# Optimization experiments

Hardware: AMD Instinct MI355X
Metric: run time of the kernel (lower is better)

The kernel has to match this reference:

```python
import jax, jax.numpy as jnp
import numpy as np


def setup_inputs() -> dict:
    key = jax.random.key(0)
    pcd = jax.random.normal(key, (8, 4096, 3), dtype=jnp.float32)
    return {"pcd": pcd, "k": 5}


def reference(pcd, k):
    # pcd: [B, N, 3]. Faithful port of MC3DAD_ONNX.get_geometry_features.
    sq = jnp.sum(pcd * pcd, axis=-1)                       # [B, N]
    d2 = sq[:, :, None] + sq[:, None, :] - 2.0 * jnp.einsum('bnd,bmd->bnm', pcd, pcd)
    dist = jnp.sqrt(jnp.maximum(d2, 0.0))                  # [B, N, N], == torch.cdist
    # k nearest neighbors (smallest distances) -> indices only
    _, idx = jax.lax.top_k(-dist, k)                       # idx: [B, N, K]
    # gather neighbor coordinates: [B, N, K, 3]
    neighbors = jax.vmap(lambda p, i: p[i])(pcd, idx)
    centroid = jnp.mean(neighbors, axis=2, keepdims=True)  # [B, N, 1, 3]
    centered = neighbors - centroid                        # [B, N, K, 3]
    # per-point 3x3 covariance: centered^T @ centered / (K-1)
    cov = jnp.einsum('bnkc,bnkd->bncd', centered, centered) / (k - 1)
    trace = jnp.trace(cov, axis1=-2, axis2=-1)             # [B, N]
    curvature = trace / (jnp.sum(trace, axis=-1, keepdims=True) + 1e-8)
    return curvature
```

## Files before the change

kernel.cpp:

```cpp
#include <hip/hip_runtime.h>
#include <hip/hip_bf16.h>


typedef unsigned long long ull;

constexpr int N_PTS  = 4096;
constexpr int BATCH  = 8;
constexpr int KNN    = 5;
constexpr int SEG    = 8;
constexpr int SEGLEN = N_PTS / SEG;
constexpr int QPW    = 8;
constexpr int NTHR   = 1024;
constexpr int QPB    = (NTHR / 64) * QPW;
constexpr int KSLOT  = 16;
constexpr int TRIG   = KSLOT - 4;

__device__ __forceinline__ int swz(int j) { return j + (j >> 9); }

__device__ __forceinline__ ull umin64(ull a, ull b) { return a < b ? a : b; }
__device__ __forceinline__ ull umax64(ull a, ull b) { return a < b ? b : a; }

__device__ __forceinline__ void push5(float dd, int idx,
                                      float d[KNN], int ix[KNN])
{
    float ad = dd; int ai = idx;
    #pragma unroll
    for (int p = 0; p < KNN - 1; ++p) {
        const bool lt = ad < d[p];
        const float md = lt ? ad : d[p];
        const int   mi = lt ? ai : ix[p];
        const float xd = lt ? d[p] : ad;
        const int   xi = lt ? ix[p] : ai;
        d[p] = md; ix[p] = mi; ad = xd; ai = xi;
    }
    const bool lt = ad < d[KNN - 1];
    d[KNN - 1]  = lt ? ad : d[KNN - 1];
    ix[KNN - 1] = lt ? ai : ix[KNN - 1];
}

__device__ __forceinline__ void merge5(ull a[KNN], const ull b[KNN])
{
    const ull r0 = umin64(a[0], b[0]);
    const ull r1 = umin64(umin64(a[1], b[1]), umax64(a[0], b[0]));
    const ull r2 = umin64(umin64(a[2], b[2]),
                          umin64(umax64(a[1], b[0]), umax64(a[0], b[1])));
    const ull r3 = umin64(umin64(a[3], b[3]),
                   umin64(umax64(a[2], b[0]),
                   umin64(umax64(a[1], b[1]), umax64(a[0], b[2]))));
    const ull r4 = umin64(umin64(a[4], b[4]),
                   umin64(umin64(umax64(a[3], b[0]), umax64(a[2], b[1])),
                          umin64(umax64(a[1], b[2]), umax64(a[0], b[3]))));
    a[0] = r0; a[1] = r1; a[2] = r2; a[3] = r3; a[4] = r4;
}

struct KnnShared {
    float4 pts[N_PTS + SEG];
    int    buf[KSLOT * NTHR];
};

__device__ __forceinline__ void drain_buf(int& cnt, const float4 qp,
                                          float dq[KNN], int iq[KNN],
                                          float& tau_q,
                                          const float4* __restrict__ pts,
                                          const int* __restrict__ lanebuf)
{
    for (int j = 0; ; ++j) {
        if (!__any(j < cnt)) break;
        if (j < cnt) {
            const int idx = lanebuf[j * NTHR];
            const float4 c = pts[swz(idx)];
            const float dot = __fadd_rn(__fadd_rn(__fmul_rn(qp.x, c.x),
                                                  __fmul_rn(qp.y, c.y)),
                                        __fmul_rn(qp.z, c.z));
            const float dd = __fsub_rn(__fadd_rn(qp.w, c.w),
                                       __fmul_rn(2.0f, dot));
            push5(dd, idx, dq, iq);
        }
    }
    cnt = 0;
    tau_q = __fsub_rn(dq[KNN - 1], qp.w) + 6e-5f;
}

__global__ __launch_bounds__(NTHR, 4)
void knn_trace_kernel(const float* __restrict__ pcd, float* __restrict__ trace_out)
{
    __shared__ KnnShared sh;

    const int b = blockIdx.y;
    const int t = threadIdx.x;
    const float* __restrict__ batch = pcd + (size_t)b * N_PTS * 3;

    #pragma unroll
    for (int i = 0; i < N_PTS / NTHR; ++i) {
        const int p = t + i * NTHR;
        const float x = batch[p * 3 + 0];
        const float y = batch[p * 3 + 1];
        const float z = batch[p * 3 + 2];
        const float sq = __fadd_rn(__fadd_rn(__fmul_rn(x, x), __fmul_rn(y, y)),
                                   __fmul_rn(z, z));
        sh.pts[swz(p)] = make_float4(x, y, z, sq);
    }
    __syncthreads();

    const int lane = t & 63;
    const int wave = t >> 6;
    const int q    = lane & 7;
    const int s    = lane >> 3;
    const int qbase = blockIdx.x * QPB + wave * QPW;
    const float4 qp = sh.pts[swz(qbase + q)];

    float dq[KNN];
    int   iq[KNN];
    #pragma unroll
    for (int r = 0; r < KNN; ++r) { dq[r] = __builtin_inff(); iq[r] = 0x7fffffff; }

    const float4* __restrict__ seg = sh.pts + (s * SEGLEN + s);
    int* __restrict__ lanebuf = sh.buf + t;

    int   cnt   = 0;
    float tau_q = __builtin_inff();
    const int idx0 = s * SEGLEN;

    for (int m0 = 0; m0 < SEGLEN; m0 += 4) {
        #pragma unroll
        for (int u = 0; u < 4; ++u) {
            const float4 c = seg[m0 + u];
            const float t2 = fmaf(-2.0f,
                                  fmaf(qp.x, c.x,
                                       fmaf(qp.y, c.y, qp.z * c.z)),
                                  c.w);
            const bool keep = t2 < tau_q;
            lanebuf[cnt * NTHR] = idx0 + m0 + u;
            cnt += keep ? 1 : 0;
        }
        if (__any(cnt > TRIG))
            drain_buf(cnt, qp, dq, iq, tau_q, sh.pts, lanebuf);
    }
    drain_buf(cnt, qp, dq, iq, tau_q, sh.pts, lanebuf);

    ull key[KNN];
    #pragma unroll
    for (int r = 0; r < KNN; ++r) {
        const float dist = __fsqrt_rn(fmaxf(dq[r], 0.0f));
        key[r] = ((ull)__float_as_uint(dist) << 32) | (unsigned)iq[r];
    }
    #pragma unroll
    for (int i = 0; i < KNN - 1; ++i)
        #pragma unroll
        for (int p = 0; p < KNN - 1 - i; ++p) {
            const ull lo = umin64(key[p], key[p + 1]);
            const ull hi = umax64(key[p], key[p + 1]);
            key[p] = lo; key[p + 1] = hi;
        }

    #pragma unroll
    for (int mask = 8; mask < 64; mask <<= 1) {
        ull o[KNN];
        #pragma unroll
        for (int r = 0; r < KNN; ++r) o[r] = __shfl_xor(key[r], mask);
        merge5(key, o);
    }

    if (lane < 8) {
        float nx[KNN], ny[KNN], nz[KNN];
        #pragma unroll
        for (int r = 0; r < KNN; ++r) {
            const int sel = (int)(key[r] & 0xffffffffull);
            const float4 p = sh.pts[swz(sel)];
            nx[r] = p.x; ny[r] = p.y; nz[r] = p.z;
        }

        float sx = nx[0], sy = ny[0], sz = nz[0];
        #pragma unroll
        for (int r = 1; r < KNN; ++r) {
            sx = __fadd_rn(sx, nx[r]);
            sy = __fadd_rn(sy, ny[r]);
            sz = __fadd_rn(sz, nz[r]);
        }
        const float cx = __fdiv_rn(sx, 5.0f);
        const float cy = __fdiv_rn(sy, 5.0f);
        const float cz = __fdiv_rn(sz, 5.0f);

        float sxx = 0.0f, syy = 0.0f, szz = 0.0f;
        #pragma unroll
        for (int r = 0; r < KNN; ++r) {
            const float dx = __fsub_rn(nx[r], cx);
            const float dy = __fsub_rn(ny[r], cy);
            const float dz = __fsub_rn(nz[r], cz);
            sxx = __fadd_rn(sxx, __fmul_rn(dx, dx));
            syy = __fadd_rn(syy, __fmul_rn(dy, dy));
            szz = __fadd_rn(szz, __fmul_rn(dz, dz));
        }
        const float trace = __fadd_rn(__fadd_rn(__fmul_rn(sxx, 0.25f),
                                                __fmul_rn(syy, 0.25f)),
                                      __fmul_rn(szz, 0.25f));
        trace_out[(size_t)b * N_PTS + qbase + lane] = trace;
    }
}

__global__ __launch_bounds__(256)
void curvature_kernel(const float* __restrict__ trace, float* __restrict__ out)
{
    __shared__ float red[256];
    const int b = blockIdx.x >> 3;
    const int c = blockIdx.x & 7;
    const int t = threadIdx.x;
    const float* __restrict__ tr = trace + (size_t)b * N_PTS;

    float s = 0.0f;
    #pragma unroll
    for (int i = 0; i < N_PTS / 256; ++i)
        s += tr[t + i * 256];
    red[t] = s;
    __syncthreads();
    #pragma unroll
    for (int o = 128; o > 0; o >>= 1) {
        if (t < o) red[t] += red[t + o];
        __syncthreads();
    }
    const float denom = red[0] + 1e-8f;

    float* __restrict__ ob = out + (size_t)b * N_PTS;
    const int x = c * 512 + t;
    ob[x]       = tr[x]       / denom;
    ob[x + 256] = tr[x + 256] / denom;
}

extern "C" void kernel_launch(void* const* d_in, const int* in_sizes, int n_in,
                              void* d_out, int out_size, void* d_ws, size_t ws_size,
                              hipStream_t stream)
{
    (void)in_sizes; (void)n_in; (void)out_size; (void)ws_size;
    const float* pcd = (const float*)d_in[0];
    float* trace = (float*)d_ws;
    float* out = (float*)d_out;

    dim3 gridA(N_PTS / QPB, BATCH);
    knn_trace_kernel<<<gridA, NTHR, 0, stream>>>(pcd, trace);
    curvature_kernel<<<BATCH * 8, 256, 0, stream>>>(trace, out);
}
```

Before: 135.5 us.

## Rewrite KNN as register-broadcast scan with shared tau and fused normalization

Replaces the shared-memory point table with per-wave register chunks that are broadcast via readlane, so each lane handles one query against a 512-point segment per wave. A running threshold is shared across waves through atomicMin on LDS. Partial top-5 lists are merged through shared memory, and the normalization kernel is folded in using a last-block-done counter. This removes the LDS point table and the second launch, but it adds a memset, global-memory gathers during drains, per-candidate wave votes, and a serial tail in the last block.

```diff
diff --git a/kernel.cpp b/kernel.cpp
--- a/kernel.cpp
+++ b/kernel.cpp
@@ -3,20 +3,23 @@
 
 
 typedef unsigned long long ull;
+typedef unsigned short u16;
+typedef unsigned int u32;
 
 constexpr int N_PTS  = 4096;
 constexpr int BATCH  = 8;
 constexpr int KNN    = 5;
-constexpr int SEG    = 8;
-constexpr int SEGLEN = N_PTS / SEG;
-constexpr int QPW    = 8;
-constexpr int NTHR   = 1024;
-constexpr int QPB    = (NTHR / 64) * QPW;
+constexpr int NTHR   = 512;
+constexpr int WPB    = 8;
+constexpr int QPB    = 64;
+constexpr int SEGLEN = 512;
+constexpr int CHUNKS = 8;
 constexpr int KSLOT  = 16;
-constexpr int TRIG   = KSLOT - 4;
-
-__device__ __forceinline__ int swz(int j) { return j + (j >> 9); }
-
+constexpr int TRIG   = 12;
+
+__device__ __forceinline__ float rl(float v, int j) {
+    return __int_as_float(__builtin_amdgcn_readlane(__float_as_int(v), j));
+}
 __device__ __forceinline__ ull umin64(ull a, ull b) { return a < b ? a : b; }
 __device__ __forceinline__ ull umax64(ull a, ull b) { return a < b ? b : a; }
 
@@ -38,7 +41,7 @@
     ix[KNN - 1] = lt ? ai : ix[KNN - 1];
 }
 
-__device__ __forceinline__ void merge5(ull a[KNN], const ull b[KNN])
+__device__ __forceinline__ void merge5(ull a[KNN], const ull* __restrict__ b)
 {
     const ull r0 = umin64(a[0], b[0]);
     const ull r1 = umin64(umin64(a[1], b[1]), umax64(a[0], b[0]));
@@ -53,90 +56,110 @@
     a[0] = r0; a[1] = r1; a[2] = r2; a[3] = r3; a[4] = r4;
 }
 
-struct KnnShared {
-    float4 pts[N_PTS + SEG];
-    int    buf[KSLOT * NTHR];
+struct Sh {
+    u16 buf[KSLOT * NTHR];
+    u32 tau_bits[QPB];
+    int lastflag;
+    union {
+        ull   mrg[QPB][WPB][KNN];
+        float red[256];
+    } u;
 };
 
-__device__ __forceinline__ void drain_buf(int& cnt, const float4 qp,
-                                          float dq[KNN], int iq[KNN],
-                                          float& tau_q,
-                                          const float4* __restrict__ pts,
-                                          const int* __restrict__ lanebuf)
-{
-    for (int j = 0; ; ++j) {
-        if (!__any(j < cnt)) break;
+__device__ __forceinline__ void drain_buf(int& cnt, float qx, float qy, float qz, float qw,
+                                          float dq[KNN], int iq[KNN], float& tau,
+                                          const float* __restrict__ batch,
+                                          const u16* lanebuf, u32* tau_bits, int lane)
+{
+    for (int j = 0; __any(j < cnt); ++j) {
         if (j < cnt) {
-            const int idx = lanebuf[j * NTHR];
-            const float4 c = pts[swz(idx)];
-            const float dot = __fadd_rn(__fadd_rn(__fmul_rn(qp.x, c.x),
-                                                  __fmul_rn(qp.y, c.y)),
-                                        __fmul_rn(qp.z, c.z));
-            const float dd = __fsub_rn(__fadd_rn(qp.w, c.w),
-                                       __fmul_rn(2.0f, dot));
+            const int idx = lanebuf[(size_t)j * NTHR];
+            const float x = batch[idx * 3 + 0];
+            const float y = batch[idx * 3 + 1];
+            const float z = batch[idx * 3 + 2];
+            const float sq  = __fadd_rn(__fadd_rn(__fmul_rn(x, x), __fmul_rn(y, y)),
+                                        __fmul_rn(z, z));
+            const float dot = __fadd_rn(__fadd_rn(__fmul_rn(qx, x), __fmul_rn(qy, y)),
+                                        __fmul_rn(qz, z));
+            const float dd  = __fsub_rn(__fadd_rn(qw, sq), __fmul_rn(2.0f, dot));
             push5(dd, idx, dq, iq);
         }
     }
     cnt = 0;
-    tau_q = __fsub_rn(dq[KNN - 1], qp.w) + 6e-5f;
+    atomicMin(&tau_bits[lane], __float_as_uint(dq[KNN - 1]));
+    const u32 tb = *(volatile u32*)&tau_bits[lane];
+    tau = __uint_as_float(tb) - qw + 6e-5f;
 }
 
 __global__ __launch_bounds__(NTHR, 4)
-void knn_trace_kernel(const float* __restrict__ pcd, float* __restrict__ trace_out)
-{
-    __shared__ KnnShared sh;
-
-    const int b = blockIdx.y;
-    const int t = threadIdx.x;
-    const float* __restrict__ batch = pcd + (size_t)b * N_PTS * 3;
-
-    #pragma unroll
-    for (int i = 0; i < N_PTS / NTHR; ++i) {
-        const int p = t + i * NTHR;
-        const float x = batch[p * 3 + 0];
-        const float y = batch[p * 3 + 1];
-        const float z = batch[p * 3 + 2];
-        const float sq = __fadd_rn(__fadd_rn(__fmul_rn(x, x), __fmul_rn(y, y)),
-                                   __fmul_rn(z, z));
-        sh.pts[swz(p)] = make_float4(x, y, z, sq);
-    }
-    __syncthreads();
-
+void fused_kernel(const float* __restrict__ pcd, float* __restrict__ out,
+                  u32* __restrict__ ctr)
+{
+    __shared__ Sh sh;
+
+    const int b    = blockIdx.y;
+    const int qb   = blockIdx.x;
+    const int t    = threadIdx.x;
     const int lane = t & 63;
     const int wave = t >> 6;
-    const int q    = lane & 7;
-    const int s    = lane >> 3;
-    const int qbase = blockIdx.x * QPB + wave * QPW;
-    const float4 qp = sh.pts[swz(qbase + q)];
-
-    float dq[KNN];
-    int   iq[KNN];
+    const float* __restrict__ batch = pcd + (size_t)b * N_PTS * 3;
+
+    if (t < QPB) sh.tau_bits[t] = 0x7f800000u;
+
+    const int q = qb * QPB + lane;
+    const float qx = batch[q * 3 + 0];
+    const float qy = batch[q * 3 + 1];
+    const float qz = batch[q * 3 + 2];
+    const float qw = __fadd_rn(__fadd_rn(__fmul_rn(qx, qx), __fmul_rn(qy, qy)),
+                               __fmul_rn(qz, qz));
+
+    const int wbase = wave * SEGLEN;
+    float cx[CHUNKS], cy[CHUNKS], cz[CHUNKS], cw[CHUNKS];
+    #pragma unroll
+    for (int c = 0; c < CHUNKS; ++c) {
+        const int idx = wbase + c * 64 + lane;
+        cx[c] = batch[idx * 3 + 0];
+        cy[c] = batch[idx * 3 + 1];
+        cz[c] = batch[idx * 3 + 2];
+        cw[c] = __fadd_rn(__fadd_rn(__fmul_rn(cx[c], cx[c]), __fmul_rn(cy[c], cy[c])),
+                          __fmul_rn(cz[c], cz[c]));
+    }
+    __syncthreads();
+
+    float dq[KNN]; int iq[KNN];
     #pragma unroll
     for (int r = 0; r < KNN; ++r) { dq[r] = __builtin_inff(); iq[r] = 0x7fffffff; }
 
-    const float4* __restrict__ seg = sh.pts + (s * SEGLEN + s);
-    int* __restrict__ lanebuf = sh.buf + t;
-
-    int   cnt   = 0;
-    float tau_q = __builtin_inff();
-    const int idx0 = s * SEGLEN;
-
-    for (int m0 = 0; m0 < SEGLEN; m0 += 4) {
-        #pragma unroll
-        for (int u = 0; u < 4; ++u) {
-            const float4 c = seg[m0 + u];
-            const float t2 = fmaf(-2.0f,
-                                  fmaf(qp.x, c.x,
-                                       fmaf(qp.y, c.y, qp.z * c.z)),
-                                  c.w);
-            const bool keep = t2 < tau_q;
-            lanebuf[cnt * NTHR] = idx0 + m0 + u;
-            cnt += keep ? 1 : 0;
-        }
-        if (__any(cnt > TRIG))
-            drain_buf(cnt, qp, dq, iq, tau_q, sh.pts, lanebuf);
-    }
-    drain_buf(cnt, qp, dq, iq, tau_q, sh.pts, lanebuf);
+    u16* lanebuf = sh.buf + t;
+    int   cnt = 0;
+    float tau = __builtin_inff();
+
+    for (int c = 0; c < CHUNKS; ++c) {
+        const u32 tb = *(volatile u32*)&sh.tau_bits[lane];
+        tau = __uint_as_float(tb) - qw + 6e-5f;
+        const int cbase = wbase + c * 64;
+        for (int j0 = 0; j0 < 64; j0 += 4) {
+            #pragma unroll
+            for (int v = 0; v < 4; ++v) {
+                const int j = j0 + v;
+                const float sx = rl(cx[c], j);
+                const float sy = rl(cy[c], j);
+                const float sz = rl(cz[c], j);
+                const float sw = rl(cw[c], j);
+                const float dot = fmaf(qx, sx, fmaf(qy, sy, qz * sz));
+                const float t2  = fmaf(-2.0f, dot, sw);
+                const bool keep = t2 < tau;
+                if (__any(keep)) {
+                    lanebuf[(size_t)cnt * NTHR] = (u16)(cbase + j);
+                    cnt += keep ? 1 : 0;
+                }
+            }
+            if (__any(cnt > TRIG))
+                drain_buf(cnt, qx, qy, qz, qw, dq, iq, tau, batch,
+                          lanebuf, sh.tau_bits, lane);
+        }
+    }
+    drain_buf(cnt, qx, qy, qz, qw, dq, iq, tau, batch, lanebuf, sh.tau_bits, lane);
 
     ull key[KNN];
     #pragma unroll
@@ -152,24 +175,25 @@
             const ull hi = umax64(key[p], key[p + 1]);
             key[p] = lo; key[p + 1] = hi;
         }
-
-    #pragma unroll
-    for (int mask = 8; mask < 64; mask <<= 1) {
-        ull o[KNN];
-        #pragma unroll
-        for (int r = 0; r < KNN; ++r) o[r] = __shfl_xor(key[r], mask);
-        merge5(key, o);
-    }
-
-    if (lane < 8) {
+    #pragma unroll
+    for (int r = 0; r < KNN; ++r) sh.u.mrg[lane][wave][r] = key[r];
+    __syncthreads();
+
+    if (wave == 0) {
+        ull cur[KNN];
+        #pragma unroll
+        for (int r = 0; r < KNN; ++r) cur[r] = sh.u.mrg[lane][0][r];
+        #pragma unroll
+        for (int w = 1; w < WPB; ++w) merge5(cur, &sh.u.mrg[lane][w][0]);
+
         float nx[KNN], ny[KNN], nz[KNN];
         #pragma unroll
         for (int r = 0; r < KNN; ++r) {
-            const int sel = (int)(key[r] & 0xffffffffull);
-            const float4 p = sh.pts[swz(sel)];
-            nx[r] = p.x; ny[r] = p.y; nz[r] = p.z;
-        }
-
+            const int sel = (int)(cur[r] & 0xffffffffull);
+            nx[r] = batch[sel * 3 + 0];
+            ny[r] = batch[sel * 3 + 1];
+            nz[r] = batch[sel * 3 + 2];
+        }
         float sx = nx[0], sy = ny[0], sz = nz[0];
         #pragma unroll
         for (int r = 1; r < KNN; ++r) {
@@ -177,16 +201,16 @@
             sy = __fadd_rn(sy, ny[r]);
             sz = __fadd_rn(sz, nz[r]);
         }
-        const float cx = __fdiv_rn(sx, 5.0f);
-        const float cy = __fdiv_rn(sy, 5.0f);
-        const float cz = __fdiv_rn(sz, 5.0f);
+        const float ccx = __fdiv_rn(sx, 5.0f);
+        const float ccy = __fdiv_rn(sy, 5.0f);
+        const float ccz = __fdiv_rn(sz, 5.0f);
 
         float sxx = 0.0f, syy = 0.0f, szz = 0.0f;
         #pragma unroll
         for (int r = 0; r < KNN; ++r) {
-            const float dx = __fsub_rn(nx[r], cx);
-            const float dy = __fsub_rn(ny[r], cy);
-            const float dz = __fsub_rn(nz[r], cz);
+            const float dx = __fsub_rn(nx[r], ccx);
+            const float dy = __fsub_rn(ny[r], ccy);
+            const float dz = __fsub_rn(nz[r], ccz);
             sxx = __fadd_rn(sxx, __fmul_rn(dx, dx));
             syy = __fadd_rn(syy, __fmul_rn(dy, dy));
             szz = __fadd_rn(szz, __fmul_rn(dz, dz));
@@ -194,36 +218,37 @@
         const float trace = __fadd_rn(__fadd_rn(__fmul_rn(sxx, 0.25f),
                                                 __fmul_rn(syy, 0.25f)),
                                       __fmul_rn(szz, 0.25f));
-        trace_out[(size_t)b * N_PTS + qbase + lane] = trace;
-    }
-}
-
-__global__ __launch_bounds__(256)
-void curvature_kernel(const float* __restrict__ trace, float* __restrict__ out)
-{
-    __shared__ float red[256];
-    const int b = blockIdx.x >> 3;
-    const int c = blockIdx.x & 7;
-    const int t = threadIdx.x;
-    const float* __restrict__ tr = trace + (size_t)b * N_PTS;
-
-    float s = 0.0f;
-    #pragma unroll
-    for (int i = 0; i < N_PTS / 256; ++i)
-        s += tr[t + i * 256];
-    red[t] = s;
-    __syncthreads();
-    #pragma unroll
-    for (int o = 128; o > 0; o >>= 1) {
-        if (t < o) red[t] += red[t + o];
+        out[(size_t)b * N_PTS + qb * QPB + lane] = trace;
+    }
+
+    __syncthreads();
+    if (t == 0) {
+        __threadfence();
+        const u32 old = atomicAdd(&ctr[b], 1u);
+        sh.lastflag = (old == (u32)(gridDim.x - 1)) ? 1 : 0;
+    }
+    __syncthreads();
+    if (sh.lastflag) {
+        __threadfence();
+        float* __restrict__ ob = out + (size_t)b * N_PTS;
+        if (t < 256) {
+            float s = 0.0f;
+            #pragma unroll
+            for (int i = 0; i < 16; ++i) s += ob[t + i * 256];
+            sh.u.red[t] = s;
+        }
         __syncthreads();
-    }
-    const float denom = red[0] + 1e-8f;
-
-    float* __restrict__ ob = out + (size_t)b * N_PTS;
-    const int x = c * 512 + t;
-    ob[x]       = tr[x]       / denom;
-    ob[x + 256] = tr[x + 256] / denom;
+        for (int o = 128; o > 0; o >>= 1) {
+            if (t < o) sh.u.red[t] += sh.u.red[t + o];
+            __syncthreads();
+        }
+        const float denom = sh.u.red[0] + 1e-8f;
+        #pragma unroll
+        for (int i = 0; i < 8; ++i) {
+            const int x = t + i * NTHR;
+            ob[x] = ob[x] / denom;
+        }
+    }
 }
 
 extern "C" void kernel_launch(void* const* d_in, const int* in_sizes, int n_in,
@@ -232,10 +257,10 @@
 {
     (void)in_sizes; (void)n_in; (void)out_size; (void)ws_size;
     const float* pcd = (const float*)d_in[0];
-    float* trace = (float*)d_ws;
     float* out = (float*)d_out;
-
-    dim3 gridA(N_PTS / QPB, BATCH);
-    knn_trace_kernel<<<gridA, NTHR, 0, stream>>>(pcd, trace);
-    curvature_kernel<<<BATCH * 8, 256, 0, stream>>>(trace, out);
-}
+    u32* ctr = (u32*)d_ws;
+
+    hipMemsetAsync(ctr, 0, BATCH * sizeof(u32), stream);
+    dim3 grid(N_PTS / QPB, BATCH);
+    fused_kernel<<<grid, NTHR, 0, stream>>>(pcd, out, ctr);
+}
```

Result: slower. 163.6 us (+20.8%).
